# Performance work log

Hardware: AMD Instinct MI355X
Metric: run time of the kernel (lower is better)

Reference implementation:

```python
import jax, jax.numpy as jnp
import numpy as np

K = 32            # spatial kernel: neighbors per anchor
STRIDE = 4        # spatial_stride -> S = N // 4 anchors
TK_HALF = 1       # temporal_kernel_size=3 -> window offsets -1,0,+1


def setup_inputs() -> dict:
    key = jax.random.key(0)
    k1, k2, k3 = jax.random.split(key, 3)
    points = jax.random.normal(k1, (2, 4, 8192, 6), dtype=jnp.float32)
    # conv_d: Conv2d(4 -> 64, 1x1, bias=False) as a dense matrix [out,in]
    Wd = jax.random.normal(k2, (64, 4), dtype=jnp.float32) * 0.1
    # mlp: Conv2d(64 -> 128, 1x1, bias=False)
    Wm = jax.random.normal(k3, (128, 64), dtype=jnp.float32) * 0.1
    return {"points": points, "Wd": Wd, "Wm": Wm}


def _fps(xyz, npoint):
    """Farthest point sampling on a single frame. xyz: [N,3] -> idx [npoint] int32.
    Deterministic start at index 0."""
    d0 = jnp.sum((xyz - xyz[0]) ** 2, axis=-1)  # [N]

    def body(dists, _):
        nxt = jnp.argmax(dists)
        d = jnp.sum((xyz - xyz[nxt]) ** 2, axis=-1)
        return jnp.minimum(dists, d), nxt.astype(jnp.int32)

    _, idxs = jax.lax.scan(body, d0, None, length=npoint - 1)
    return jnp.concatenate([jnp.zeros((1,), jnp.int32), idxs])


def _knn_idx(neighbor_xyz, anchor_xyz, k):
    """Adaptive ball query realized as k-nearest-neighbors.
    neighbor_xyz: [B,N,3], anchor_xyz: [B,S,3] -> idx [B,S,k]."""
    d2 = jnp.sum((anchor_xyz[:, :, None, :] - neighbor_xyz[:, None, :, :]) ** 2, axis=-1)  # [B,S,N]
    _, idx = jax.lax.top_k(-d2, k)
    return idx


def _group(pts, idx):
    """pts: [B,N,C], idx: [B,S,K] -> [B,S,K,C] gather per batch."""
    return jax.vmap(lambda p, i: p[i])(pts, idx)


def reference(points, Wd, Wm):
    xyzs = points[..., :3]                       # [B,L,N,3] (rgb unused when in_planes==0)
    B, L, N, _ = xyzs.shape
    S = N // STRIDE
    # replicate temporal padding [1,1]
    pad = jnp.concatenate([xyzs[:, :1], xyzs, xyzs[:, -1:]], axis=1)  # [B,L+2,N,3]

    new_xyzs, new_feats = [], []
    for t in range(TK_HALF, L + 2 - TK_HALF):    # anchor frames in padded indexing
        frame = pad[:, t]                        # [B,N,3]
        aidx = jax.vmap(lambda x: _fps(x, S))(frame)       # [B,S]
        anchor = _group(frame, aidx[:, :, None])[:, :, 0]  # [B,S,3]

        fsum = jnp.zeros((B, S, Wm.shape[0]), dtype=points.dtype)
        for di in range(-TK_HALF, TK_HALF + 1):
            nb = pad[:, t + di]                              # [B,N,3]
            idx = _knn_idx(nb, anchor, K)                    # [B,S,K]
            grouped = _group(nb, idx)                        # [B,S,K,3]
            disp = grouped - anchor[:, :, None, :]           # xyz displacement
            tdisp = jnp.full((B, S, K, 1), float(di), dtype=points.dtype)
            d4 = jnp.concatenate([disp, tdisp], axis=-1)     # [B,S,K,4]
            h = jax.nn.relu(jnp.einsum('bskc,oc->bsko', d4, Wd))   # conv_d + ReLU
            h = jax.nn.relu(jnp.einsum('bsko,po->bskp', h, Wm))    # mlp + ReLU
            fsum = fsum + jnp.max(h, axis=2)                 # spatial max-pool, temporal sum
        new_xyzs.append(anchor)
        new_feats.append(fsum)

    new_xyzs = jnp.stack(new_xyzs, axis=1)                   # [B,T,S,3]
    new_feats = jnp.stack(new_feats, axis=1).transpose(0, 1, 3, 2)  # [B,T,C,S]
    return new_xyzs, new_feats
```

## Files before the change

### kernel.cpp

```cpp
#include <hip/hip_runtime.h>
#include <stdint.h>

#define NPTS 8192
#define NS   2048
#define KNNK 32

typedef unsigned long long u64;
typedef float f32x2 __attribute__((ext_vector_type(2)));

__device__ __forceinline__ float wave_max_f32_dpp(float x) {
    int t;
    t = __builtin_amdgcn_update_dpp(0, __float_as_int(x), 0xB1, 0xF, 0xF, false);
    x = fmaxf(x, __int_as_float(t));
    t = __builtin_amdgcn_update_dpp(0, __float_as_int(x), 0x4E, 0xF, 0xF, false);
    x = fmaxf(x, __int_as_float(t));
    t = __builtin_amdgcn_update_dpp(0, __float_as_int(x), 0x141, 0xF, 0xF, false);
    x = fmaxf(x, __int_as_float(t));
    t = __builtin_amdgcn_update_dpp(0, __float_as_int(x), 0x140, 0xF, 0xF, false);
    x = fmaxf(x, __int_as_float(t));
    t = __builtin_amdgcn_update_dpp(0, __float_as_int(x), 0x142, 0xF, 0xF, false);
    x = fmaxf(x, __int_as_float(t));
    t = __builtin_amdgcn_update_dpp(0, __float_as_int(x), 0x143, 0xF, 0xF, false);
    x = fmaxf(x, __int_as_float(t));
    return x;
}

__device__ __forceinline__ int wave_min_i32_dpp(int x) {
    const int INF = 0x7FFFFFFF;
    int t;
    t = __builtin_amdgcn_update_dpp(INF, x, 0xB1, 0xF, 0xF, false);
    x = t < x ? t : x;
    t = __builtin_amdgcn_update_dpp(INF, x, 0x4E, 0xF, 0xF, false);
    x = t < x ? t : x;
    t = __builtin_amdgcn_update_dpp(INF, x, 0x141, 0xF, 0xF, false);
    x = t < x ? t : x;
    t = __builtin_amdgcn_update_dpp(INF, x, 0x140, 0xF, 0xF, false);
    x = t < x ? t : x;
    t = __builtin_amdgcn_update_dpp(INF, x, 0x142, 0xF, 0xF, false);
    x = t < x ? t : x;
    t = __builtin_amdgcn_update_dpp(INF, x, 0x143, 0xF, 0xF, false);
    x = t < x ? t : x;
    return x;
}

__global__ __launch_bounds__(512)
void fps_kernel(const float* __restrict__ pts,
                float* __restrict__ out_xyz)
{
#pragma clang fp contract(off)
    const int bt  = blockIdx.x;
    const int tid = threadIdx.x;
    const float* frame = pts + (size_t)bt * NPTS * 6;

    __shared__ float4 p4[NPTS];
    __shared__ float wmaxs[8];
    __shared__ unsigned selIdx[2];

    f32x2 x2[8], y2[8], z2[8], dd2[8];
#pragma unroll
    for (int j = 0; j < 16; ++j) {
        int n = j * 512 + tid;
        float x = frame[n*6+0], y = frame[n*6+1], z = frame[n*6+2];
        x2[j >> 1][j & 1] = x;
        y2[j >> 1][j & 1] = y;
        z2[j >> 1][j & 1] = z;
        dd2[j >> 1][j & 1] = 3.4028234663852886e38f;
        p4[n] = make_float4(x, y, z, 0.0f);
    }
    if (tid < 2) selIdx[tid] = 0x7FFFFFFFu;
    if (tid == 0) {
        float* ow = out_xyz + (size_t)bt * NS * 3;
        ow[0] = x2[0][0]; ow[1] = y2[0][0]; ow[2] = z2[0][0];
    }
    __syncthreads();
    float sx = p4[0].x, sy = p4[0].y, sz = p4[0].z;

    for (int i = 1; i < NS; ++i) {
        const int pi = i & 1;
        f32x2 sxv = {sx, sx}, syv = {sy, sy}, szv = {sz, sz};
        f32x2 m2 = {0.0f, 0.0f};
#pragma unroll
        for (int q = 0; q < 8; ++q) {
            f32x2 dx = x2[q] - sxv;
            f32x2 dy = y2[q] - syv;
            f32x2 dz = z2[q] - szv;
            f32x2 dd = (dx*dx + dy*dy) + dz*dz;
            f32x2 nd;
            nd[0] = fminf(dd2[q][0], dd[0]);
            nd[1] = fminf(dd2[q][1], dd[1]);
            dd2[q] = nd;
            m2[0] = fmaxf(m2[0], nd[0]);
            m2[1] = fmaxf(m2[1], nd[1]);
        }
        float mloc = fmaxf(m2[0], m2[1]);
        float wM = wave_max_f32_dpp(mloc);
        if ((tid & 63) == 63) wmaxs[tid >> 6] = wM;
        __syncthreads();
        float4 w0 = *(const float4*)&wmaxs[0];
        float4 w1 = *(const float4*)&wmaxs[4];
        float M = fmaxf(fmaxf(fmaxf(w0.x, w0.y), fmaxf(w0.z, w0.w)),
                        fmaxf(fmaxf(w1.x, w1.y), fmaxf(w1.z, w1.w)));
        bool match = (mloc == M);
        if (__any(match)) {
            unsigned mask = 0;
#pragma unroll
            for (int j = 0; j < 16; ++j)
                mask |= (dd2[j >> 1][j & 1] == M) ? (1u << j) : 0u;
            int bestn = mask ? (int)(__builtin_ctz(mask) * 512 + tid)
                             : 0x7FFFFFFF;
            int wI = wave_min_i32_dpp(bestn);
            if ((tid & 63) == 63) atomicMin(&selIdx[pi], (unsigned)wI);
        }
        __syncthreads();
        unsigned idx = selIdx[pi];
        if (tid == 0) selIdx[pi ^ 1] = 0x7FFFFFFFu;
        float4 c = p4[idx];
        sx = c.x; sy = c.y; sz = c.z;
        if (tid == 0) {
            float* ow = out_xyz + ((size_t)bt * NS + i) * 3;
            ow[0] = sx; ow[1] = sy; ow[2] = sz;
        }
    }
}

__device__ __forceinline__ void knn_compact(u64* st, int lane, int& cnt, u64& rk)
{
    for (int e = 0; e < 32; ++e)
        if (e >= cnt) st[(e + 32) * 64 + lane] = ~0ull;
    for (int k = 2; k <= 32; k <<= 1)
        for (int j = k >> 1; j > 0; j >>= 1)
            for (int i = 0; i < 32; ++i) {
                int l = i ^ j;
                if (l > i) {
                    u64 a = st[(i + 32) * 64 + lane];
                    u64 b = st[(l + 32) * 64 + lane];
                    bool asc = ((i & k) == 0);
                    if ((a > b) == asc) {
                        st[(i + 32) * 64 + lane] = b;
                        st[(l + 32) * 64 + lane] = a;
                    }
                }
            }
    for (int i = 0; i < 32; ++i) {
        u64 a = st[i * 64 + lane];
        u64 b = st[(63 - i) * 64 + lane];
        if (b < a) st[i * 64 + lane] = b;
    }
    for (int j = 16; j > 0; j >>= 1)
        for (int i = 0; i < 32; ++i) {
            int l = i ^ j;
            if (l > i) {
                u64 a = st[i * 64 + lane];
                u64 b = st[l * 64 + lane];
                if (a > b) {
                    st[i * 64 + lane] = b;
                    st[l * 64 + lane] = a;
                }
            }
        }
    rk = st[31 * 64 + lane];
    cnt = 0;
}

__global__ __launch_bounds__(64)
void knn_kernel(const float* __restrict__ pts,
                const float* __restrict__ anchors,
                unsigned short* __restrict__ knn_out)
{
    const int blk  = blockIdx.x;
    const int bt   = blk / 96;
    const int r    = blk % 96;
    const int di   = r / 32;
    const int sblk = r % 32;
    const int b = bt >> 2, t0 = bt & 3;
    int lnb = t0 + di - 1; lnb = lnb < 0 ? 0 : (lnb > 3 ? 3 : lnb);
    const float* nb = pts + (size_t)(b * 4 + lnb) * NPTS * 6;
    const int lane = threadIdx.x;
    const int s    = sblk * 64 + lane;

    const float* ap = anchors + ((size_t)bt * NS + s) * 3;
    float ax = ap[0], ay = ap[1], az = ap[2];

    __shared__ u64 st[65 * 64];
    __shared__ float4 tile[512];

    for (int e = 0; e < 64; ++e) st[e * 64 + lane] = ~0ull;
    u64 rk = ~0ull;
    int cnt = 0;

    for (int tb = 0; tb < NPTS; tb += 512) {
        __syncthreads();
#pragma unroll
        for (int q = 0; q < 8; ++q) {
            int c = q * 64 + lane;
            int n = tb + c;
            tile[c] = make_float4(nb[n*6+0], nb[n*6+1], nb[n*6+2], 0.0f);
        }
        __syncthreads();
        for (int c0 = 0; c0 < 512; c0 += 8) {
#pragma unroll
            for (int j = 0; j < 8; ++j) {
                float4 qv = tile[c0 + j];
                float dx = __fsub_rn(ax, qv.x);
                float dy = __fsub_rn(ay, qv.y);
                float dz = __fsub_rn(az, qv.z);
                float d2 = __fadd_rn(__fadd_rn(__fmul_rn(dx,dx), __fmul_rn(dy,dy)),
                                     __fmul_rn(dz,dz));
                u64 key = ((u64)__float_as_uint(d2) << 32)
                        | (unsigned)(tb + c0 + j);
                bool p = key < rk;
                int row = p ? (32 + cnt) : 64;
                st[row * 64 + lane] = key;
                cnt += p ? 1 : 0;
            }
            if (__any(cnt >= 24)) knn_compact(st, lane, cnt, rk);
        }
    }
    knn_compact(st, lane, cnt, rk);

    unsigned short* op = knn_out + (((size_t)bt * 3 + di) * NS + s) * KNNK;
#pragma unroll
    for (int e = 0; e < 32; ++e)
        op[e] = (unsigned short)(st[e * 64 + lane] & 0xFFFFull);
}

__global__ __launch_bounds__(256)
void mlp_kernel(const float* __restrict__ pts,
                const float* __restrict__ anchors,
                const unsigned short* __restrict__ knn,
                const float* __restrict__ Wd,
                const float* __restrict__ Wm,
                float* __restrict__ out_feats)
{
    const int blk   = blockIdx.x;
    const int bt    = blk >> 10;
    const int spair = blk & 1023;
    const int b = bt >> 2, t0 = bt & 3;
    const int tid = threadIdx.x;
    const int a   = tid >> 7;
    const int r   = tid & 127;
    const int pt  = r & 31;
    const int kt  = r >> 5;
    const int p   = r;
    const int s   = spair * 2 + a;
    const int p0  = pt * 4, k0 = kt * 8;

    __shared__ float WmT[64 * 128];
    __shared__ float Wds[256];
    __shared__ float h1[2][64][32];
    __shared__ float d4s[2][32][4];
    __shared__ float pmax[2][4][128];

    for (int i = tid; i < 8192; i += 256) {
        int pp = i >> 6, oo = i & 63;
        WmT[oo * 128 + pp] = Wm[i];
    }
    Wds[tid & 255] = Wd[tid & 255];

    float fsum = 0.0f;

    for (int dd = 0; dd < 3; ++dd) {
        __syncthreads();
        if (tid < 64) {
            int sa = tid >> 5, k = tid & 31;
            int ss = spair * 2 + sa;
            int lnb = t0 + dd - 1; lnb = lnb < 0 ? 0 : (lnb > 3 ? 3 : lnb);
            const float* nbf = pts + (size_t)(b*4 + lnb) * NPTS * 6;
            const float* ap = anchors + ((size_t)bt * NS + ss) * 3;
            int idx = knn[(((size_t)bt*3 + dd) * NS + ss) * KNNK + k];
            d4s[sa][k][0] = nbf[idx*6+0] - ap[0];
            d4s[sa][k][1] = nbf[idx*6+1] - ap[1];
            d4s[sa][k][2] = nbf[idx*6+2] - ap[2];
            d4s[sa][k][3] = (float)(dd - 1);
        }
        __syncthreads();
        {
            int k  = tid & 31;
            int oq = (tid >> 5) & 3;
            float4 dv = *(const float4*)&d4s[a][k][0];
#pragma unroll
            for (int ii = 0; ii < 16; ++ii) {
                int o = oq * 16 + ii;
                float4 w = *(const float4*)&Wds[o * 4];
                float h = fmaf(dv.x, w.x, fmaf(dv.y, w.y, fmaf(dv.z, w.z, dv.w * w.w)));
                h1[a][o][k] = fmaxf(h, 0.0f);
            }
        }
        __syncthreads();
        float acc[4][8];
#pragma unroll
        for (int i = 0; i < 4; ++i)
#pragma unroll
            for (int j = 0; j < 8; ++j) acc[i][j] = 0.0f;
        for (int o = 0; o < 64; ++o) {
            float4 wv = *(const float4*)&WmT[o * 128 + p0];
            float4 h0 = *(const float4*)&h1[a][o][k0];
            float4 h4 = *(const float4*)&h1[a][o][k0 + 4];
#pragma unroll
            for (int i = 0; i < 4; ++i) {
                float w = (i == 0) ? wv.x : (i == 1) ? wv.y : (i == 2) ? wv.z : wv.w;
                acc[i][0] = fmaf(w, h0.x, acc[i][0]);
                acc[i][1] = fmaf(w, h0.y, acc[i][1]);
                acc[i][2] = fmaf(w, h0.z, acc[i][2]);
                acc[i][3] = fmaf(w, h0.w, acc[i][3]);
                acc[i][4] = fmaf(w, h4.x, acc[i][4]);
                acc[i][5] = fmaf(w, h4.y, acc[i][5]);
                acc[i][6] = fmaf(w, h4.z, acc[i][6]);
                acc[i][7] = fmaf(w, h4.w, acc[i][7]);
            }
        }
        float4 pm;
#pragma unroll
        for (int i = 0; i < 4; ++i) {
            float m = acc[i][0];
#pragma unroll
            for (int j = 1; j < 8; ++j) m = fmaxf(m, acc[i][j]);
            ((float*)&pm)[i] = m;
        }
        *(float4*)&pmax[a][kt][p0] = pm;
        __syncthreads();
        float m = fmaxf(fmaxf(pmax[a][0][p], pmax[a][1][p]),
                        fmaxf(pmax[a][2][p], pmax[a][3][p]));
        fsum += fmaxf(m, 0.0f);
    }
    out_feats[((size_t)bt * 128 + p) * NS + s] = fsum;
}

extern "C" void kernel_launch(void* const* d_in, const int* in_sizes, int n_in,
                              void* d_out, int out_size, void* d_ws, size_t ws_size,
                              hipStream_t stream)
{
    const float* pts = (const float*)d_in[0];
    const float* Wd  = (const float*)d_in[1];
    const float* Wm  = (const float*)d_in[2];

    float* out_xyz   = (float*)d_out;
    float* out_feats = out_xyz + 8 * NS * 3;

    unsigned short* knn = (unsigned short*)d_ws;

    fps_kernel<<<8, 512, 0, stream>>>(pts, out_xyz);
    knn_kernel<<<8 * 3 * 32, 64, 0, stream>>>(pts, out_xyz, knn);
    mlp_kernel<<<8 * (NS / 2), 256, 0, stream>>>(pts, out_xyz, knn, Wd, Wm, out_feats);
}
```

Measured before the change: 3.087 ms.

## Split KNN candidate scan across two waves, defer FPS coordinate writes

The KNN kernel now runs two waves per anchor block. Each wave scans half of the neighbor points straight from global memory, with no shared tile, keeps its own top-32 list, and the two sorted lists are merged at the end. The pruning threshold becomes a float distance compare, and compaction triggers at 16 pending candidates instead of 24. FPS records the selected indices in shared memory and writes all anchor coordinates in one pass after the loop, removing the serial per-iteration global stores. This doubles the parallelism of the KNN phase, at the cost of more shared memory per block and uncached uniform global loads.

```diff
diff --git a/kernel.cpp b/kernel.cpp
--- a/kernel.cpp
+++ b/kernel.cpp
@@ -53,6 +53,7 @@
     const float* frame = pts + (size_t)bt * NPTS * 6;
 
     __shared__ float4 p4[NPTS];
+    __shared__ unsigned short selidx[NS];
     __shared__ float wmaxs[8];
     __shared__ unsigned selIdx[2];
 
@@ -68,10 +69,7 @@
         p4[n] = make_float4(x, y, z, 0.0f);
     }
     if (tid < 2) selIdx[tid] = 0x7FFFFFFFu;
-    if (tid == 0) {
-        float* ow = out_xyz + (size_t)bt * NS * 3;
-        ow[0] = x2[0][0]; ow[1] = y2[0][0]; ow[2] = z2[0][0];
-    }
+    if (tid == 0) selidx[0] = 0;
     __syncthreads();
     float sx = p4[0].x, sy = p4[0].y, sz = p4[0].z;
 
@@ -113,17 +111,23 @@
         }
         __syncthreads();
         unsigned idx = selIdx[pi];
-        if (tid == 0) selIdx[pi ^ 1] = 0x7FFFFFFFu;
+        if (tid == 0) {
+            selIdx[pi ^ 1] = 0x7FFFFFFFu;
+            selidx[i] = (unsigned short)idx;
+        }
         float4 c = p4[idx];
         sx = c.x; sy = c.y; sz = c.z;
-        if (tid == 0) {
-            float* ow = out_xyz + ((size_t)bt * NS + i) * 3;
-            ow[0] = sx; ow[1] = sy; ow[2] = sz;
-        }
-    }
-}
-
-__device__ __forceinline__ void knn_compact(u64* st, int lane, int& cnt, u64& rk)
+    }
+    __syncthreads();
+    float* ow = out_xyz + (size_t)bt * NS * 3;
+    for (int t = tid; t < NS * 3; t += 512) {
+        int ii = t / 3, c = t - ii * 3;
+        float4 pc = p4[selidx[ii]];
+        ow[t] = (c == 0) ? pc.x : (c == 1) ? pc.y : pc.z;
+    }
+}
+
+__device__ __forceinline__ void knn_compact(u64* st, int lane, int& cnt, float& rk_f)
 {
     for (int e = 0; e < 32; ++e)
         if (e >= cnt) st[(e + 32) * 64 + lane] = ~0ull;
@@ -158,11 +162,11 @@
                 }
             }
         }
-    rk = st[31 * 64 + lane];
+    rk_f = __uint_as_float((unsigned)(st[31 * 64 + lane] >> 32));
     cnt = 0;
 }
 
-__global__ __launch_bounds__(64)
+__global__ __launch_bounds__(128)
 void knn_kernel(const float* __restrict__ pts,
                 const float* __restrict__ anchors,
                 unsigned short* __restrict__ knn_out)
@@ -175,53 +179,53 @@
     const int b = bt >> 2, t0 = bt & 3;
     int lnb = t0 + di - 1; lnb = lnb < 0 ? 0 : (lnb > 3 ? 3 : lnb);
     const float* nb = pts + (size_t)(b * 4 + lnb) * NPTS * 6;
-    const int lane = threadIdx.x;
+    const int tid  = threadIdx.x;
+    const int w    = tid >> 6;
+    const int lane = tid & 63;
     const int s    = sblk * 64 + lane;
 
     const float* ap = anchors + ((size_t)bt * NS + s) * 3;
     float ax = ap[0], ay = ap[1], az = ap[2];
 
-    __shared__ u64 st[65 * 64];
-    __shared__ float4 tile[512];
-
-    for (int e = 0; e < 64; ++e) st[e * 64 + lane] = ~0ull;
-    u64 rk = ~0ull;
+    __shared__ u64 st[2][65 * 64];
+    u64* stw = st[w];
+
+    for (int e = 0; e < 64; ++e) stw[e * 64 + lane] = ~0ull;
+    float rk_f = __uint_as_float(0x7F800000u);
     int cnt = 0;
 
-    for (int tb = 0; tb < NPTS; tb += 512) {
-        __syncthreads();
-#pragma unroll
-        for (int q = 0; q < 8; ++q) {
-            int c = q * 64 + lane;
-            int n = tb + c;
-            tile[c] = make_float4(nb[n*6+0], nb[n*6+1], nb[n*6+2], 0.0f);
-        }
-        __syncthreads();
-        for (int c0 = 0; c0 < 512; c0 += 8) {
-#pragma unroll
-            for (int j = 0; j < 8; ++j) {
-                float4 qv = tile[c0 + j];
-                float dx = __fsub_rn(ax, qv.x);
-                float dy = __fsub_rn(ay, qv.y);
-                float dz = __fsub_rn(az, qv.z);
-                float d2 = __fadd_rn(__fadd_rn(__fmul_rn(dx,dx), __fmul_rn(dy,dy)),
-                                     __fmul_rn(dz,dz));
-                u64 key = ((u64)__float_as_uint(d2) << 32)
-                        | (unsigned)(tb + c0 + j);
-                bool p = key < rk;
-                int row = p ? (32 + cnt) : 64;
-                st[row * 64 + lane] = key;
-                cnt += p ? 1 : 0;
-            }
-            if (__any(cnt >= 24)) knn_compact(st, lane, cnt, rk);
-        }
-    }
-    knn_compact(st, lane, cnt, rk);
-
-    unsigned short* op = knn_out + (((size_t)bt * 3 + di) * NS + s) * KNNK;
-#pragma unroll
-    for (int e = 0; e < 32; ++e)
-        op[e] = (unsigned short)(st[e * 64 + lane] & 0xFFFFull);
+    const int cbase = w * 4096;
+    for (int tb = 0; tb < 4096; tb += 16) {
+#pragma unroll
+        for (int j = 0; j < 16; ++j) {
+            int n = cbase + tb + j;
+            float qx = nb[n*6+0], qy = nb[n*6+1], qz = nb[n*6+2];
+            float dx = __fsub_rn(ax, qx);
+            float dy = __fsub_rn(ay, qy);
+            float dz = __fsub_rn(az, qz);
+            float d2 = __fadd_rn(__fadd_rn(__fmul_rn(dx,dx), __fmul_rn(dy,dy)),
+                                 __fmul_rn(dz,dz));
+            bool p = !(d2 > rk_f);
+            int row = p ? (32 + cnt) : 64;
+            stw[row * 64 + lane] =
+                ((u64)__float_as_uint(d2) << 32) | (unsigned)n;
+            cnt += p ? 1 : 0;
+        }
+        if (__any(cnt >= 16)) knn_compact(stw, lane, cnt, rk_f);
+    }
+    knn_compact(stw, lane, cnt, rk_f);
+    __syncthreads();
+
+    if (w == 0) {
+        unsigned short* op = knn_out + (((size_t)bt * 3 + di) * NS + s) * KNNK;
+#pragma unroll
+        for (int e = 0; e < 32; ++e) {
+            u64 a = st[0][e * 64 + lane];
+            u64 c = st[1][(31 - e) * 64 + lane];
+            u64 m = c < a ? c : a;
+            op[e] = (unsigned short)(m & 0xFFFFull);
+        }
+    }
 }
 
 __global__ __launch_bounds__(256)
@@ -298,15 +302,15 @@
             float4 h4 = *(const float4*)&h1[a][o][k0 + 4];
 #pragma unroll
             for (int i = 0; i < 4; ++i) {
-                float w = (i == 0) ? wv.x : (i == 1) ? wv.y : (i == 2) ? wv.z : wv.w;
-                acc[i][0] = fmaf(w, h0.x, acc[i][0]);
-                acc[i][1] = fmaf(w, h0.y, acc[i][1]);
-                acc[i][2] = fmaf(w, h0.z, acc[i][2]);
-                acc[i][3] = fmaf(w, h0.w, acc[i][3]);
-                acc[i][4] = fmaf(w, h4.x, acc[i][4]);
-                acc[i][5] = fmaf(w, h4.y, acc[i][5]);
-                acc[i][6] = fmaf(w, h4.z, acc[i][6]);
-                acc[i][7] = fmaf(w, h4.w, acc[i][7]);
+                float w2 = (i == 0) ? wv.x : (i == 1) ? wv.y : (i == 2) ? wv.z : wv.w;
+                acc[i][0] = fmaf(w2, h0.x, acc[i][0]);
+                acc[i][1] = fmaf(w2, h0.y, acc[i][1]);
+                acc[i][2] = fmaf(w2, h0.z, acc[i][2]);
+                acc[i][3] = fmaf(w2, h0.w, acc[i][3]);
+                acc[i][4] = fmaf(w2, h4.x, acc[i][4]);
+                acc[i][5] = fmaf(w2, h4.y, acc[i][5]);
+                acc[i][6] = fmaf(w2, h4.z, acc[i][6]);
+                acc[i][7] = fmaf(w2, h4.w, acc[i][7]);
             }
         }
         float4 pm;
@@ -340,6 +344,6 @@
     unsigned short* knn = (unsigned short*)d_ws;
 
     fps_kernel<<<8, 512, 0, stream>>>(pts, out_xyz);
-    knn_kernel<<<8 * 3 * 32, 64, 0, stream>>>(pts, out_xyz, knn);
+    knn_kernel<<<8 * 3 * 32, 128, 0, stream>>>(pts, out_xyz, knn);
     mlp_kernel<<<8 * (NS / 2), 256, 0, stream>>>(pts, out_xyz, knn, Wd, Wm, out_feats);
 }
```

After: 3.273 ms. +6.0%, slower.

## Use packed 64-bit atomicMax argmax with triple-buffered slot in FPS loop

Applied to the files above, without the earlier changes.

The FPS iteration previously needed two block barriers: one to share per-wave maxima and one to resolve the argmax index via atomicMin. Now each wave packs its max distance and inverted index into a 64-bit key and does a single shared atomicMax, with a three-slot ring so clearing the next slot needs no extra barrier, leaving one barrier per iteration. Output coordinates are deferred: selected indices go to shared memory and are written out coalesced after the loop. Tie-breaking keeps the lowest index through the inverted-index encoding, which relies on distances being non-negative so their float bits order like unsigned integers.

```diff
diff --git a/kernel.cpp b/kernel.cpp
--- a/kernel.cpp
+++ b/kernel.cpp
@@ -53,8 +53,8 @@
     const float* frame = pts + (size_t)bt * NPTS * 6;
 
     __shared__ float4 p4[NPTS];
-    __shared__ float wmaxs[8];
-    __shared__ unsigned selIdx[2];
+    __shared__ unsigned short selidx[NS];
+    __shared__ u64 ring[3];
 
     f32x2 x2[8], y2[8], z2[8], dd2[8];
 #pragma unroll
@@ -67,16 +67,13 @@
         dd2[j >> 1][j & 1] = 3.4028234663852886e38f;
         p4[n] = make_float4(x, y, z, 0.0f);
     }
-    if (tid < 2) selIdx[tid] = 0x7FFFFFFFu;
-    if (tid == 0) {
-        float* ow = out_xyz + (size_t)bt * NS * 3;
-        ow[0] = x2[0][0]; ow[1] = y2[0][0]; ow[2] = z2[0][0];
-    }
+    if (tid < 3) ring[tid] = 0;
+    if (tid == 0) selidx[0] = 0;
     __syncthreads();
     float sx = p4[0].x, sy = p4[0].y, sz = p4[0].z;
 
+    int r = 1;
     for (int i = 1; i < NS; ++i) {
-        const int pi = i & 1;
         f32x2 sxv = {sx, sx}, syv = {sy, sy}, szv = {sz, sz};
         f32x2 m2 = {0.0f, 0.0f};
 #pragma unroll
@@ -94,32 +91,34 @@
         }
         float mloc = fmaxf(m2[0], m2[1]);
         float wM = wave_max_f32_dpp(mloc);
-        if ((tid & 63) == 63) wmaxs[tid >> 6] = wM;
-        __syncthreads();
-        float4 w0 = *(const float4*)&wmaxs[0];
-        float4 w1 = *(const float4*)&wmaxs[4];
-        float M = fmaxf(fmaxf(fmaxf(w0.x, w0.y), fmaxf(w0.z, w0.w)),
-                        fmaxf(fmaxf(w1.x, w1.y), fmaxf(w1.z, w1.w)));
-        bool match = (mloc == M);
-        if (__any(match)) {
-            unsigned mask = 0;
-#pragma unroll
-            for (int j = 0; j < 16; ++j)
-                mask |= (dd2[j >> 1][j & 1] == M) ? (1u << j) : 0u;
-            int bestn = mask ? (int)(__builtin_ctz(mask) * 512 + tid)
-                             : 0x7FFFFFFF;
-            int wI = wave_min_i32_dpp(bestn);
-            if ((tid & 63) == 63) atomicMin(&selIdx[pi], (unsigned)wI);
-        }
-        __syncthreads();
-        unsigned idx = selIdx[pi];
-        if (tid == 0) selIdx[pi ^ 1] = 0x7FFFFFFFu;
+        float wMb = __int_as_float(
+            __builtin_amdgcn_readlane(__float_as_int(wM), 63));
+        int bestn = 0x7FFFFFFF;
+#pragma unroll
+        for (int j = 15; j >= 0; --j)
+            bestn = (dd2[j >> 1][j & 1] == wMb) ? (j * 512 + tid) : bestn;
+        int wI = wave_min_i32_dpp(bestn);
+        if ((tid & 63) == 63) {
+            u64 key = ((u64)__float_as_uint(wMb) << 32)
+                    | (unsigned)(8191 - wI);
+            atomicMax(&ring[r], key);
+        }
+        int rn = r + 1; if (rn == 3) rn = 0;
+        if (tid == 0) ring[rn] = 0;
+        __syncthreads();
+        u64 k = ring[r];
+        int idx = 8191 - (int)(k & 0xFFFFFFFFu);
+        if (tid == 0) selidx[i] = (unsigned short)idx;
         float4 c = p4[idx];
         sx = c.x; sy = c.y; sz = c.z;
-        if (tid == 0) {
-            float* ow = out_xyz + ((size_t)bt * NS + i) * 3;
-            ow[0] = sx; ow[1] = sy; ow[2] = sz;
-        }
+        r = rn;
+    }
+    __syncthreads();
+    float* ow = out_xyz + (size_t)bt * NS * 3;
+    for (int t = tid; t < NS * 3; t += 512) {
+        int ii = t / 3, c = t - ii * 3;
+        float4 pc = p4[selidx[ii]];
+        ow[t] = (c == 0) ? pc.x : (c == 1) ? pc.y : pc.z;
     }
 }
 
@@ -298,15 +297,15 @@
             float4 h4 = *(const float4*)&h1[a][o][k0 + 4];
 #pragma unroll
             for (int i = 0; i < 4; ++i) {
-                float w = (i == 0) ? wv.x : (i == 1) ? wv.y : (i == 2) ? wv.z : wv.w;
-                acc[i][0] = fmaf(w, h0.x, acc[i][0]);
-                acc[i][1] = fmaf(w, h0.y, acc[i][1]);
-                acc[i][2] = fmaf(w, h0.z, acc[i][2]);
-                acc[i][3] = fmaf(w, h0.w, acc[i][3]);
-                acc[i][4] = fmaf(w, h4.x, acc[i][4]);
-                acc[i][5] = fmaf(w, h4.y, acc[i][5]);
-                acc[i][6] = fmaf(w, h4.z, acc[i][6]);
-                acc[i][7] = fmaf(w, h4.w, acc[i][7]);
+                float w2 = (i == 0) ? wv.x : (i == 1) ? wv.y : (i == 2) ? wv.z : wv.w;
+                acc[i][0] = fmaf(w2, h0.x, acc[i][0]);
+                acc[i][1] = fmaf(w2, h0.y, acc[i][1]);
+                acc[i][2] = fmaf(w2, h0.z, acc[i][2]);
+                acc[i][3] = fmaf(w2, h0.w, acc[i][3]);
+                acc[i][4] = fmaf(w2, h4.x, acc[i][4]);
+                acc[i][5] = fmaf(w2, h4.y, acc[i][5]);
+                acc[i][6] = fmaf(w2, h4.z, acc[i][6]);
+                acc[i][7] = fmaf(w2, h4.w, acc[i][7]);
             }
         }
         float4 pm;
```

Measured after the change: 3.039 ms. Within noise of the previous version (-1.5%).
